# Performance work log

Hardware: AMD Instinct MI355X
Metric: run time of the kernel (lower is better)

## Reference

```python
import jax, jax.numpy as jnp
import numpy as np

K0 = 16                       # probe slice length (hard-coded in kernel)
TAU = 2.053748910631823       # t-test threshold (|tau| of kernel constant)


def setup_inputs() -> dict:
    key = jax.random.key(0)
    k1, k2, k3 = jax.random.split(key, 3)
    B, DIN, DOUT = 8192, 4096, 4096
    x = jax.random.normal(k1, (B, DIN), dtype=jnp.float32)
    W = jax.random.normal(k2, (DOUT, DIN), dtype=jnp.float32)
    bias = jax.random.normal(k3, (DOUT,), dtype=jnp.float32)
    return {"x": x, "W": W, "bias": bias}


def reference(x, W, bias):
    # --- partial dot over the first K0 columns of K (the probe) ---
    x0 = x[:, :K0]                    # [B, K0]
    w0 = W[:, :K0]                    # [DOUT, K0]
    y1 = x0 @ w0.T                    # [B, DOUT]  sum_k x_k * w_k
    # sum of squared elementwise products: prod_k^2 = x_k^2 * w_k^2
    s2 = (x0 * x0) @ (w0 * w0).T      # [B, DOUT]
    # --- per-(row, column) t-statistic and early-exit decision ---
    tstat = jnp.abs(y1) / jnp.sqrt(s2 / K0)
    passed = tstat < TAU              # True -> column deemed insignificant, zeroed
    # --- full linear (active columns keep full accumulation + bias) ---
    full = x @ W.T + bias[None, :]    # [B, DOUT]
    return jnp.where(passed, 0.0, full)
```

## Files before the change

kernel.cpp:

```cpp
#include <hip/hip_runtime.h>
#include <cstdint>
#include <cstddef>

#define TAU_D 2.053748910631823
#define M_DIM 8192
#define N_DIM 4096
#define K_DIM 4096
#define NT32  (K_DIM / 32)

typedef float f32x4  __attribute__((ext_vector_type(4)));
typedef short bf16x8 __attribute__((ext_vector_type(8)));

typedef __attribute__((address_space(1))) void gvoid_t;
typedef __attribute__((address_space(3))) void lvoid_t;

__device__ __forceinline__ void gload_lds16(const void* g, void* l) {
    __builtin_amdgcn_global_load_lds((const gvoid_t*)g, (lvoid_t*)l, 16, 0, 0);
}

__device__ __forceinline__ unsigned int pack2bf(float lo, float hi) {
    unsigned int ul = __float_as_uint(lo);
    unsigned int uh = __float_as_uint(hi);
    ul = (ul + 0x7FFFu + ((ul >> 16) & 1u)) >> 16;
    uh = (uh + 0x7FFFu + ((uh >> 16) & 1u)) >> 16;
    return ul | (uh << 16);
}

__global__ void cvt_f32_to_bf16(const float4* __restrict__ in,
                                uint2* __restrict__ out, int n4) {
    int i = blockIdx.x * blockDim.x + threadIdx.x;
    const int stride = gridDim.x * blockDim.x;
    for (; i < n4; i += stride) {
        float4 a = in[i];
        uint2 o;
        o.x = pack2bf(a.x, a.y);
        o.y = pack2bf(a.z, a.w);
        out[i] = o;
    }
}

#define BAR() do { __builtin_amdgcn_s_barrier(); \
                   asm volatile("" ::: "memory"); } while (0)

__global__ __launch_bounds__(512, 2) void gemm_masked8(
    const unsigned short* __restrict__ Ab,
    const unsigned short* __restrict__ Bb,
    const float* __restrict__ X,
    const float* __restrict__ Wt,
    const float* __restrict__ bias,
    float* __restrict__ out)
{
    __shared__ __align__(16) char lds[98304];

    const int tid  = threadIdx.x;
    const int wave = tid >> 6;
    const int lane = tid & 63;
    const int lr = lane & 15;
    const int lq = lane >> 4;
    const int wm = wave >> 2;
    const int wn = wave & 3;

    const int flat = blockIdx.x;
    const int xcd  = flat & 7;
    const int s    = flat >> 3;
    const int rnd  = s >> 5;
    const int jj   = s & 31;
    const int trow = rnd * 16 + ((xcd >> 2) << 3) + (jj >> 2);
    const int tcol = ((xcd & 3) << 2) + (jj & 3);
    const int rowBase = trow * 256;
    const int colBase = tcol * 256;

    f32x4 acc[8][4];
    #pragma unroll
    for (int i = 0; i < 8; ++i)
        #pragma unroll
        for (int n = 0; n < 4; ++n)
            acc[i][n] = (f32x4){0.f, 0.f, 0.f, 0.f};

    const int srow = tid >> 2;
    const int slog = ((tid & 3) - ((tid >> 3) & 3)) & 3;
    const unsigned short* aSrc =
        Ab + (size_t)(rowBase + srow) * K_DIM + slog * 8;
    const unsigned short* bSrc =
        Bb + (size_t)(colBase + srow) * K_DIM + slog * 8;

    auto stageK = [&](int kst, unsigned bo) {
        #pragma unroll
        for (int i = 0; i < 2; ++i)
            gload_lds16(aSrc + (size_t)i * 128 * K_DIM + kst * 32,
                        lds + bo + i * 8192 + wave * 1024);
        #pragma unroll
        for (int i = 0; i < 2; ++i)
            gload_lds16(bSrc + (size_t)i * 128 * K_DIM + kst * 32,
                        lds + bo + 16384 + i * 8192 + wave * 1024);
    };

    const unsigned skrot = (unsigned)((lq + (lr >> 1)) & 3) * 16;
    const unsigned offA0 = (unsigned)(wm * 128 + lr) * 64 + skrot;
    const unsigned offB0 = 16384u + (unsigned)(wn * 64 + lr) * 64 + skrot;

    stageK(0, 0);
    stageK(1, 32768);
    asm volatile("s_waitcnt vmcnt(4)" ::: "memory");
    BAR();

    unsigned b0 = 0, b1 = 32768, b2 = 65536;

    for (int T = 0; T < NT32; ++T) {
        const char* L = lds + b0;

        bf16x8 bF[4], aq[4];

        #pragma unroll
        for (int n = 0; n < 4; ++n)
            bF[n] = *(const bf16x8*)(L + offB0 + n * 1024);
        #pragma unroll
        for (int m = 0; m < 4; ++m)
            aq[m] = *(const bf16x8*)(L + offA0 + m * 1024);
        if (T + 2 < NT32) stageK(T + 2, b2);

        __builtin_amdgcn_s_setprio(1);
        #pragma unroll
        for (int m = 0; m < 4; ++m)
            #pragma unroll
            for (int n = 0; n < 4; ++n)
                acc[m][n] = __builtin_amdgcn_mfma_f32_16x16x32_bf16(
                    aq[m], bF[n], acc[m][n], 0, 0, 0);
        __builtin_amdgcn_s_setprio(0);

        #pragma unroll
        for (int m = 0; m < 4; ++m)
            aq[m] = *(const bf16x8*)(L + offA0 + (4 + m) * 1024);
        __builtin_amdgcn_s_setprio(1);
        #pragma unroll
        for (int m = 0; m < 4; ++m)
            #pragma unroll
            for (int n = 0; n < 4; ++n)
                acc[4 + m][n] = __builtin_amdgcn_mfma_f32_16x16x32_bf16(
                    aq[m], bF[n], acc[4 + m][n], 0, 0, 0);
        __builtin_amdgcn_s_setprio(0);

        if (T + 2 < NT32) {
            asm volatile("s_waitcnt vmcnt(4)" ::: "memory");
        } else if (T + 1 < NT32) {
            asm volatile("s_waitcnt vmcnt(0)" ::: "memory");
        }
        BAR();

        unsigned t = b0; b0 = b1; b1 = b2; b2 = t;
    }

    __syncthreads();
    float* x0s = (float*)(lds);
    float* w0s = (float*)(lds + 16384);
    #pragma unroll
    for (int i = 0; i < 2; ++i) {
        int idx = tid + i * 512;
        int r = idx >> 2, qq = (idx & 3) << 2;
        *(f32x4*)(x0s + r * 16 + qq) =
            *(const f32x4*)(X + (size_t)(rowBase + r) * K_DIM + qq);
        *(f32x4*)(w0s + r * 16 + qq) =
            *(const f32x4*)(Wt + (size_t)(colBase + r) * K_DIM + qq);
    }
    __syncthreads();

    const float TAU32 = (float)TAU_D;

    #pragma unroll
    for (int np = 0; np < 4; np += 2) {
        float wv[2][16];
        float bv[2];
        #pragma unroll
        for (int e = 0; e < 2; ++e) {
            const int c = wn * 64 + (np + e) * 16 + lr;
            #pragma unroll
            for (int q = 0; q < 4; ++q)
                *(f32x4*)&wv[e][q * 4] = *(const f32x4*)(w0s + c * 16 + q * 4);
            bv[e] = bias[colBase + c];
        }
        #pragma unroll
        for (int mi = 0; mi < 8; ++mi) {
            #pragma unroll
            for (int jr = 0; jr < 4; ++jr) {
                const int rw = wm * 128 + mi * 16 + lq * 4 + jr;
                float xv[16];
                #pragma unroll
                for (int q = 0; q < 4; ++q)
                    *(f32x4*)&xv[q * 4] = *(const f32x4*)(x0s + rw * 16 + q * 4);
                const size_t orow = (size_t)(rowBase + rw) * N_DIM + colBase;
                #pragma unroll
                for (int e = 0; e < 2; ++e) {
                    const int n = np + e;
                    float y1 = 0.f, s2 = 0.f;
                    #pragma unroll
                    for (int k = 0; k < 16; ++k) {
                        float xk = xv[k], wk = wv[e][k];
                        float xx = xk * xk, ww = wk * wk;
                        y1 = fmaf(xk, wk, y1);
                        s2 = fmaf(xx, ww, s2);
                    }
                    float t = fabsf(y1) / sqrtf(s2 * 0.0625f);
                    float v = (t < TAU32) ? 0.0f : (acc[mi][n][jr] + bv[e]);
                    out[orow + wn * 64 + n * 16 + lr] = v;
                }
            }
        }
    }
}

__global__ __launch_bounds__(256, 2) void gemm_masked_fb(
    const float* __restrict__ X, const float* __restrict__ Wt,
    const float* __restrict__ bias, float* __restrict__ out)
{
    __shared__ __align__(16) unsigned short As[128 * 32];
    __shared__ __align__(16) unsigned short Bs[128 * 32];

    const int tid  = threadIdx.x;
    const int wave = tid >> 6;
    const int lane = tid & 63;
    const int rowBase = blockIdx.y * 128;
    const int colBase = blockIdx.x * 128;
    const int wr = wave >> 1;
    const int wc = wave & 1;
    const int lr = lane & 15;
    const int lq = lane >> 4;

    f32x4 acc[4][4];
    #pragma unroll
    for (int m = 0; m < 4; ++m)
        #pragma unroll
        for (int n = 0; n < 4; ++n)
            acc[m][n] = (f32x4){0.f, 0.f, 0.f, 0.f};

    const int srow = tid >> 2;
    const int scol = (tid & 3) * 8;
    const float* afp = X  + (size_t)(rowBase + srow) * K_DIM + scol;
    const float* bfp = Wt + (size_t)(colBase + srow) * K_DIM + scol;

    for (int kt = 0; kt < K_DIM; kt += 32) {
        #pragma unroll
        for (int issue = 0; issue < 2; ++issue) {
            const float* sa = afp + (size_t)issue * 64 * K_DIM;
            const float* sb = bfp + (size_t)issue * 64 * K_DIM;
            float4 a0 = *(const float4*)(sa);
            float4 a1 = *(const float4*)(sa + 4);
            float4 b0 = *(const float4*)(sb);
            float4 b1 = *(const float4*)(sb + 4);
            uint4 pa, pb;
            pa.x = pack2bf(a0.x, a0.y); pa.y = pack2bf(a0.z, a0.w);
            pa.z = pack2bf(a1.x, a1.y); pa.w = pack2bf(a1.z, a1.w);
            pb.x = pack2bf(b0.x, b0.y); pb.y = pack2bf(b0.z, b0.w);
            pb.z = pack2bf(b1.x, b1.y); pb.w = pack2bf(b1.z, b1.w);
            *(uint4*)((char*)As + issue * 4096 + tid * 16) = pa;
            *(uint4*)((char*)Bs + issue * 4096 + tid * 16) = pb;
        }
        afp += 32; bfp += 32;
        __syncthreads();

        bf16x8 af[4], bq[4];
        #pragma unroll
        for (int m = 0; m < 4; ++m)
            af[m] = *(const bf16x8*)(As + (wr * 64 + m * 16 + lr) * 32 + lq * 8);
        #pragma unroll
        for (int n = 0; n < 4; ++n)
            bq[n] = *(const bf16x8*)(Bs + (wc * 64 + n * 16 + lr) * 32 + lq * 8);
        #pragma unroll
        for (int m = 0; m < 4; ++m)
            #pragma unroll
            for (int n = 0; n < 4; ++n)
                acc[m][n] = __builtin_amdgcn_mfma_f32_16x16x32_bf16(
                    af[m], bq[n], acc[m][n], 0, 0, 0);
        __syncthreads();
    }

    float* x0s = (float*)As;
    float* w0s = (float*)Bs;
    #pragma unroll
    for (int i = 0; i < 2; ++i) {
        int idx = tid + i * 256;
        int r = idx >> 2, q = (idx & 3) * 4;
        *(float4*)(x0s + r * 16 + q) =
            *(const float4*)(X + (size_t)(rowBase + r) * K_DIM + q);
        *(float4*)(w0s + r * 16 + q) =
            *(const float4*)(Wt + (size_t)(colBase + r) * K_DIM + q);
    }
    __syncthreads();

    const float TAU32 = (float)TAU_D;
    float wv[4][16];
    float bv[4];
    #pragma unroll
    for (int n = 0; n < 4; ++n) {
        int c = wc * 64 + n * 16 + lr;
        #pragma unroll
        for (int q = 0; q < 4; ++q)
            *(f32x4*)&wv[n][q * 4] = *(const f32x4*)(w0s + c * 16 + q * 4);
        bv[n] = bias[colBase + c];
    }

    #pragma unroll
    for (int m = 0; m < 4; ++m) {
        #pragma unroll
        for (int j = 0; j < 4; ++j) {
            const int r = wr * 64 + m * 16 + lq * 4 + j;
            float xv[16];
            #pragma unroll
            for (int q = 0; q < 4; ++q)
                *(f32x4*)&xv[q * 4] = *(const f32x4*)(x0s + r * 16 + q * 4);
            const size_t orow = (size_t)(rowBase + r) * N_DIM + colBase;
            #pragma unroll
            for (int n = 0; n < 4; ++n) {
                float y1 = 0.f, s2 = 0.f;
                #pragma unroll
                for (int k = 0; k < 16; ++k) {
                    float xk = xv[k];
                    float wk = wv[n][k];
                    float xx = xk * xk;
                    float ww = wk * wk;
                    y1 = fmaf(xk, wk, y1);
                    s2 = fmaf(xx, ww, s2);
                }
                float t = fabsf(y1) / sqrtf(s2 * 0.0625f);
                float v = (t < TAU32) ? 0.0f : (acc[m][n][j] + bv[n]);
                out[orow + wc * 64 + n * 16 + lr] = v;
            }
        }
    }
}

extern "C" void kernel_launch(void* const* d_in, const int* in_sizes, int n_in,
                              void* d_out, int out_size, void* d_ws, size_t ws_size,
                              hipStream_t stream) {
    const float* x    = (const float*)d_in[0];
    const float* W    = (const float*)d_in[1];
    const float* bias = (const float*)d_in[2];
    float* out = (float*)d_out;

    const size_t needA = (size_t)M_DIM * K_DIM * 2;
    const size_t needB = (size_t)N_DIM * K_DIM * 2;

    if (ws_size >= needA + needB) {
        unsigned short* xb = (unsigned short*)d_ws;
        unsigned short* wb = (unsigned short*)((char*)d_ws + needA);
        cvt_f32_to_bf16<<<2048, 256, 0, stream>>>(
            (const float4*)x, (uint2*)xb, (M_DIM * K_DIM) / 4);
        cvt_f32_to_bf16<<<2048, 256, 0, stream>>>(
            (const float4*)W, (uint2*)wb, (N_DIM * K_DIM) / 4);
        dim3 grid((M_DIM / 256) * (N_DIM / 256));
        gemm_masked8<<<grid, 512, 0, stream>>>(xb, wb, x, W, bias, out);
    } else {
        dim3 grid(N_DIM / 128, M_DIM / 128);
        gemm_masked_fb<<<grid, 256, 0, stream>>>(x, W, bias, out);
    }
}
```

Before: 334.4 us.

## Shrink GEMM block tile to 256x128 with 4x2 wave grid for higher occupancy

Halves the block's N tile from 256 to 128 columns, rearranges the 8 waves into a 4x2 grid each computing 64x64, and cuts LDS per block from 96KB to 72KB. It also raises launch bounds to 4 blocks per SM and doubles the grid, remapping the XCD tile swizzle to match. The aim is more resident blocks and halved accumulator registers to hide latency better. The cost is lower arithmetic intensity per LDS byte and per global load, since A tiles are reloaded twice as often.

```diff
diff --git a/kernel.cpp b/kernel.cpp
--- a/kernel.cpp
+++ b/kernel.cpp
@@ -42,7 +42,7 @@
 #define BAR() do { __builtin_amdgcn_s_barrier(); \
                    asm volatile("" ::: "memory"); } while (0)
 
-__global__ __launch_bounds__(512, 2) void gemm_masked8(
+__global__ __launch_bounds__(512, 4) void gemm_masked8(
     const unsigned short* __restrict__ Ab,
     const unsigned short* __restrict__ Bb,
     const float* __restrict__ X,
@@ -50,29 +50,29 @@
     const float* __restrict__ bias,
     float* __restrict__ out)
 {
-    __shared__ __align__(16) char lds[98304];
+    __shared__ __align__(16) char lds[73728];
 
     const int tid  = threadIdx.x;
     const int wave = tid >> 6;
     const int lane = tid & 63;
     const int lr = lane & 15;
     const int lq = lane >> 4;
-    const int wm = wave >> 2;
-    const int wn = wave & 3;
+    const int wm = wave >> 1;
+    const int wn = wave & 1;
 
     const int flat = blockIdx.x;
     const int xcd  = flat & 7;
     const int s    = flat >> 3;
-    const int rnd  = s >> 5;
-    const int jj   = s & 31;
-    const int trow = rnd * 16 + ((xcd >> 2) << 3) + (jj >> 2);
-    const int tcol = ((xcd & 3) << 2) + (jj & 3);
+    const int rnd  = s >> 6;
+    const int jj   = s & 63;
+    const int trow = rnd * 16 + ((xcd >> 2) << 3) + (jj >> 3);
+    const int tcol = ((xcd & 3) << 3) + (jj & 7);
     const int rowBase = trow * 256;
-    const int colBase = tcol * 256;
-
-    f32x4 acc[8][4];
-    #pragma unroll
-    for (int i = 0; i < 8; ++i)
+    const int colBase = tcol * 128;
+
+    f32x4 acc[4][4];
+    #pragma unroll
+    for (int i = 0; i < 4; ++i)
         #pragma unroll
         for (int n = 0; n < 4; ++n)
             acc[i][n] = (f32x4){0.f, 0.f, 0.f, 0.f};
@@ -89,34 +89,30 @@
         for (int i = 0; i < 2; ++i)
             gload_lds16(aSrc + (size_t)i * 128 * K_DIM + kst * 32,
                         lds + bo + i * 8192 + wave * 1024);
-        #pragma unroll
-        for (int i = 0; i < 2; ++i)
-            gload_lds16(bSrc + (size_t)i * 128 * K_DIM + kst * 32,
-                        lds + bo + 16384 + i * 8192 + wave * 1024);
+        gload_lds16(bSrc + kst * 32, lds + bo + 16384 + wave * 1024);
     };
 
-    const unsigned skrot = (unsigned)((lq + (lr >> 1)) & 3) * 16;
-    const unsigned offA0 = (unsigned)(wm * 128 + lr) * 64 + skrot;
-    const unsigned offB0 = 16384u + (unsigned)(wn * 64 + lr) * 64 + skrot;
+    const unsigned rot  = (unsigned)((lq + (lr >> 1)) & 3) * 16;
+    const unsigned offA = (unsigned)(wm * 64 + lr) * 64 + rot;
+    const unsigned offB = 16384u + (unsigned)(wn * 64 + lr) * 64 + rot;
 
     stageK(0, 0);
-    stageK(1, 32768);
-    asm volatile("s_waitcnt vmcnt(4)" ::: "memory");
+    stageK(1, 24576);
+    asm volatile("s_waitcnt vmcnt(3)" ::: "memory");
     BAR();
 
-    unsigned b0 = 0, b1 = 32768, b2 = 65536;
+    unsigned b0 = 0, b1 = 24576, b2 = 49152;
 
     for (int T = 0; T < NT32; ++T) {
         const char* L = lds + b0;
 
-        bf16x8 bF[4], aq[4];
-
+        bf16x8 aF[4], bF[4];
+        #pragma unroll
+        for (int m = 0; m < 4; ++m)
+            aF[m] = *(const bf16x8*)(L + offA + m * 1024);
         #pragma unroll
         for (int n = 0; n < 4; ++n)
-            bF[n] = *(const bf16x8*)(L + offB0 + n * 1024);
-        #pragma unroll
-        for (int m = 0; m < 4; ++m)
-            aq[m] = *(const bf16x8*)(L + offA0 + m * 1024);
+            bF[n] = *(const bf16x8*)(L + offB + n * 1024);
         if (T + 2 < NT32) stageK(T + 2, b2);
 
         __builtin_amdgcn_s_setprio(1);
@@ -125,23 +121,11 @@
             #pragma unroll
             for (int n = 0; n < 4; ++n)
                 acc[m][n] = __builtin_amdgcn_mfma_f32_16x16x32_bf16(
-                    aq[m], bF[n], acc[m][n], 0, 0, 0);
+                    aF[m], bF[n], acc[m][n], 0, 0, 0);
         __builtin_amdgcn_s_setprio(0);
 
-        #pragma unroll
-        for (int m = 0; m < 4; ++m)
-            aq[m] = *(const bf16x8*)(L + offA0 + (4 + m) * 1024);
-        __builtin_amdgcn_s_setprio(1);
-        #pragma unroll
-        for (int m = 0; m < 4; ++m)
-            #pragma unroll
-            for (int n = 0; n < 4; ++n)
-                acc[4 + m][n] = __builtin_amdgcn_mfma_f32_16x16x32_bf16(
-                    aq[m], bF[n], acc[4 + m][n], 0, 0, 0);
-        __builtin_amdgcn_s_setprio(0);
-
         if (T + 2 < NT32) {
-            asm volatile("s_waitcnt vmcnt(4)" ::: "memory");
+            asm volatile("s_waitcnt vmcnt(3)" ::: "memory");
         } else if (T + 1 < NT32) {
             asm volatile("s_waitcnt vmcnt(0)" ::: "memory");
         }
@@ -159,6 +143,9 @@
         int r = idx >> 2, qq = (idx & 3) << 2;
         *(f32x4*)(x0s + r * 16 + qq) =
             *(const f32x4*)(X + (size_t)(rowBase + r) * K_DIM + qq);
+    }
+    {
+        int r = tid >> 2, qq = (tid & 3) << 2;
         *(f32x4*)(w0s + r * 16 + qq) =
             *(const f32x4*)(Wt + (size_t)(colBase + r) * K_DIM + qq);
     }
@@ -179,10 +166,10 @@
             bv[e] = bias[colBase + c];
         }
         #pragma unroll
-        for (int mi = 0; mi < 8; ++mi) {
+        for (int mi = 0; mi < 4; ++mi) {
             #pragma unroll
             for (int jr = 0; jr < 4; ++jr) {
-                const int rw = wm * 128 + mi * 16 + lq * 4 + jr;
+                const int rw = wm * 64 + mi * 16 + lq * 4 + jr;
                 float xv[16];
                 #pragma unroll
                 for (int q = 0; q < 4; ++q)
@@ -346,7 +333,7 @@
             (const float4*)x, (uint2*)xb, (M_DIM * K_DIM) / 4);
         cvt_f32_to_bf16<<<2048, 256, 0, stream>>>(
             (const float4*)W, (uint2*)wb, (N_DIM * K_DIM) / 4);
-        dim3 grid((M_DIM / 256) * (N_DIM / 256));
+        dim3 grid((M_DIM / 256) * (N_DIM / 128));
         gemm_masked8<<<grid, 512, 0, stream>>>(xb, wb, x, W, bias, out);
     } else {
         dim3 grid(N_DIM / 128, M_DIM / 128);
```

After: 415.1 us. 1.24x slower.
